# Kernel optimization log

Hardware: AMD Instinct MI355X
Metric: run time of the kernel (lower is better)

The kernel has to match this reference:

```python
import jax, jax.numpy as jnp
import numpy as np
from jax import lax

HEADS = 8
DIM_HEAD = 64
INNER = HEADS * DIM_HEAD  # 512
LOG_SCALE_MAX = float(np.log(100.0))  # clamp for clamp_exp (SwinV2-style max temperature 1/0.01)
EPS_NORM = 1e-12  # F.normalize eps
EPS_LN = 1e-5


def setup_inputs() -> dict:
    key = jax.random.key(0)
    ks = jax.random.split(key, 6)
    b, c, h, w = 2, 256, 48, 48
    x = jax.random.normal(ks[0], (b, c, h, w), jnp.float32)
    w_in = jax.random.normal(ks[1], (3 * INNER, c), jnp.float32) * (c ** -0.5)
    b_in = jnp.zeros((3 * INNER,), jnp.float32)
    # learnable log-scale, init log(d_head ** -0.5), per head
    softmax_scale = jnp.full((HEADS, 1, 1), float(np.log(DIM_HEAD ** -0.5)), jnp.float32)
    w_dw = jax.random.normal(ks[2], (INNER, 1, 3, 3), jnp.float32) * (1.0 / 3.0)
    w_pw = jax.random.normal(ks[3], (2 * c, INNER), jnp.float32) * (INNER ** -0.5)
    gamma = jnp.full((2 * c,), 1e-3, jnp.float32)  # norm init_weight=0.001
    beta = jnp.zeros((2 * c,), jnp.float32)
    return {"x": x, "w_in": w_in, "b_in": b_in, "softmax_scale": softmax_scale,
            "w_dw": w_dw, "w_pw": w_pw, "gamma": gamma, "beta": beta}


def _l2norm(t):
    n = jnp.sqrt(jnp.sum(t * t, axis=-1, keepdims=True))
    return t / jnp.maximum(n, EPS_NORM)


def reference(x, w_in, b_in, softmax_scale, w_dw, w_pw, gamma, beta):
    b, c, h, w = x.shape
    s = h * w
    # proj_in: 1x1 conv then 'b (h c) x y -> b h x y c'
    y = jnp.einsum('bchw,oc->bohw', x, w_in) + b_in[None, :, None, None]
    y = y.reshape(b, HEADS, 3 * DIM_HEAD, h, w).transpose(0, 1, 3, 4, 2)  # b H x y (3*dh)
    y = y.reshape(b, HEADS, s, 3 * DIM_HEAD)
    q, k, v = jnp.split(y, 3, axis=-1)  # each [b, H, s, dh]
    # scaled cosine attention
    qn, kn = _l2norm(q), _l2norm(k)
    scale = jnp.exp(jnp.minimum(softmax_scale, LOG_SCALE_MAX))  # clamp_exp, [H,1,1]
    sim = jnp.einsum('bhid,bhjd->bhij', qn, kn) * scale[None]
    attn = jax.nn.softmax(sim, axis=-1)
    out = jnp.einsum('bhij,bhjd->bhid', attn, v)  # [b,H,s,dh]
    # unsplit heads -> 'b (h w) c' -> 'b c h w'
    update = out.transpose(0, 2, 1, 3).reshape(b, s, INNER)
    update = update.transpose(0, 2, 1).reshape(b, INNER, h, w)
    # proj_out: depthwise 3x3 (no bias) + pointwise 1x1 (no bias)
    dw = lax.conv_general_dilated(update, w_dw, (1, 1), 'SAME',
                                  feature_group_count=INNER,
                                  dimension_numbers=('NCHW', 'OIHW', 'NCHW'))
    pw = jnp.einsum('bchw,oc->bohw', dw, w_pw)  # [b, 2c, h, w]
    # channelwise layernorm with small init weight (norm_scales_and_shifts)
    mu = jnp.mean(pw, axis=1, keepdims=True)
    var = jnp.var(pw, axis=1, keepdims=True)
    normed = (pw - mu) * lax.rsqrt(var + EPS_LN)
    normed = normed * gamma[None, :, None, None] + beta[None, :, None, None]
    scales, shifts = jnp.split(normed, 2, axis=1)  # each [b, c, h, w]
    return shifts + x * scales
```

## Files before the change

### kernel.cpp

```cpp
#include <hip/hip_runtime.h>

#define B_ 2
#define C_ 256
#define S_ 2304
#define DH_ 64
#define O3_ 1536
#define INNER_ 512
#define LOGSMAX 4.605170185988092f
#define LOG2E 1.4426950408889634f

typedef __attribute__((ext_vector_type(8))) short short8;
typedef __attribute__((ext_vector_type(4))) float f32x4;
typedef __attribute__((ext_vector_type(16))) float f32x16;
typedef __attribute__((ext_vector_type(4))) unsigned short us4;
typedef __attribute__((ext_vector_type(2))) unsigned u32x2;
typedef __attribute__((ext_vector_type(4))) unsigned u32x4;
typedef __bf16 bf16x8 __attribute__((ext_vector_type(8)));

__device__ __forceinline__ unsigned short f2bf(float f) {
  unsigned u = __builtin_bit_cast(unsigned, f);
  u += 0x7FFFu + ((u >> 16) & 1u);
  return (unsigned short)(u >> 16);
}
__device__ __forceinline__ float bf2f(unsigned short h) {
  return __builtin_bit_cast(float, (unsigned)h << 16);
}
__device__ __forceinline__ bf16x8 as_bf(short8 v) {
  return __builtin_bit_cast(bf16x8, v);
}
__device__ __forceinline__ float fexp2(float x) {
#if __has_builtin(__builtin_amdgcn_exp2f)
  return __builtin_amdgcn_exp2f(x);
#else
  return __expf(x * 0.6931471805599453f);
#endif
}
__device__ __forceinline__ float frcp(float x) {
#if __has_builtin(__builtin_amdgcn_rcpf)
  return __builtin_amdgcn_rcpf(x);
#else
  return 1.f / x;
#endif
}
__device__ __forceinline__ unsigned pack_hi16(unsigned b, unsigned a) {
  return __builtin_amdgcn_perm(b, a, 0x07060302u);
}
__device__ __forceinline__ unsigned pack_lo16(unsigned b, unsigned a) {
  return __builtin_amdgcn_perm(b, a, 0x05040100u);
}

__global__ __launch_bounds__(256) void k_prep(const float* __restrict__ x,
                                              const float* __restrict__ w_in,
                                              const float* __restrict__ w_pw,
                                              unsigned short* __restrict__ xT,
                                              unsigned short* __restrict__ w_inb,
                                              unsigned short* __restrict__ w_pwb) {
  __shared__ float tile[64][65];
  int blk = blockIdx.x;
  int t = threadIdx.x;
  if (blk < 288) {
    int p0 = (blk % 36) * 64, c0 = ((blk / 36) % 4) * 64, b = blk / 144;
    const float* xb = x + (size_t)b * C_ * S_;
#pragma unroll
    for (int i = 0; i < 16; i++) {
      int c = i * 4 + (t >> 6);
      int p = t & 63;
      tile[c][p] = xb[(size_t)(c0 + c) * S_ + p0 + p];
    }
    __syncthreads();
    unsigned short* xTb = xT + (size_t)b * S_ * C_;
#pragma unroll
    for (int i = 0; i < 16; i++) {
      int p = i * 4 + (t >> 6);
      int c = t & 63;
      xTb[(size_t)(p0 + p) * C_ + c0 + c] = f2bf(tile[c][p]);
    }
  } else if (blk < 288 + 1536) {
    int i = (blk - 288) * 256 + t;
    w_inb[i] = f2bf(w_in[i]);
  } else {
    int i = (blk - 1824) * 256 + t;
    w_pwb[i] = f2bf(w_pw[i]);
  }
}

__global__ __launch_bounds__(256) void k_gemm_qkv(const unsigned short* __restrict__ A,
                                                  const unsigned short* __restrict__ BT,
                                                  const float* __restrict__ b_in,
                                                  const float* __restrict__ ss,
                                                  unsigned char* __restrict__ qn,
                                                  unsigned char* __restrict__ kn,
                                                  unsigned short* __restrict__ vv) {
  __shared__ __align__(16) unsigned short As[64][72];
  __shared__ __align__(16) unsigned short Bs[128][72];
  int t = threadIdx.x;
  int lane = t & 63, wv = t >> 6;
  int quad = lane >> 4, r15 = lane & 15;
  int by = blockIdx.y;
  int m0 = by * 64, n0 = blockIdx.x * 128;
  int b = blockIdx.z;
  const unsigned short* BTb = BT + (size_t)b * S_ * C_;

  f32x4 acc[4][2] = {};

  int srA = t >> 2, scA = (t & 3) * 16;
  int srB = t >> 1, scB = (t & 1) * 32;
  const unsigned short* ag = A + (size_t)(m0 + srA) * C_ + scA;
  const unsigned short* bg = BTb + (size_t)(n0 + srB) * C_ + scB;

  for (int k0 = 0; k0 < C_; k0 += 64) {
    short8 a0 = *(const short8*)(ag + k0);
    short8 a1 = *(const short8*)(ag + k0 + 8);
    short8 b0 = *(const short8*)(bg + k0);
    short8 b1 = *(const short8*)(bg + k0 + 8);
    short8 b2 = *(const short8*)(bg + k0 + 16);
    short8 b3 = *(const short8*)(bg + k0 + 24);
    __syncthreads();
    *(short8*)&As[srA][scA] = a0;
    *(short8*)&As[srA][scA + 8] = a1;
    *(short8*)&Bs[srB][scB] = b0;
    *(short8*)&Bs[srB][scB + 8] = b1;
    *(short8*)&Bs[srB][scB + 16] = b2;
    *(short8*)&Bs[srB][scB + 24] = b3;
    __syncthreads();
#pragma unroll
    for (int ks = 0; ks < 2; ks++) {
      short8 af[4], bfr[2];
#pragma unroll
      for (int i = 0; i < 4; i++) af[i] = *(const short8*)&As[i * 16 + r15][ks * 32 + quad * 8];
#pragma unroll
      for (int j = 0; j < 2; j++) bfr[j] = *(const short8*)&Bs[wv * 32 + j * 16 + r15][ks * 32 + quad * 8];
#pragma unroll
      for (int i = 0; i < 4; i++)
#pragma unroll
        for (int j = 0; j < 2; j++)
          acc[i][j] = __builtin_amdgcn_mfma_f32_16x16x32_bf16(as_bf(af[i]), as_bf(bfr[j]), acc[i][j], 0, 0, 0);
    }
  }

  int h = by / 3, seg = by - h * 3;
  int bh = b * 8 + h;
  f32x4 bi[4];
#pragma unroll
  for (int i = 0; i < 4; i++) bi[i] = *(const f32x4*)&b_in[m0 + i * 16 + quad * 4];
  float bv[4][2][4];
  float ssq0 = 0.f, ssq1 = 0.f;
#pragma unroll
  for (int i = 0; i < 4; i++)
#pragma unroll
    for (int rr = 0; rr < 4; rr++) {
      float v0 = acc[i][0][rr] + bi[i][rr];
      float v1 = acc[i][1][rr] + bi[i][rr];
      bv[i][0][rr] = v0;
      bv[i][1][rr] = v1;
      ssq0 += v0 * v0;
      ssq1 += v1 * v1;
    }
  if (seg < 2) {
    float sc = (seg == 0) ? __expf(fminf(ss[h], LOGSMAX)) * LOG2E : 1.f;
    ssq0 += __shfl_xor(ssq0, 16);
    ssq0 += __shfl_xor(ssq0, 32);
    ssq1 += __shfl_xor(ssq1, 16);
    ssq1 += __shfl_xor(ssq1, 32);
    float inv0 = sc / fmaxf(sqrtf(ssq0), 1e-12f);
    float inv1 = sc / fmaxf(sqrtf(ssq1), 1e-12f);
    unsigned char* dst = (seg == 0 ? qn : kn) + (size_t)bh * S_ * DH_;
#pragma unroll
    for (int i = 0; i < 4; i++)
#pragma unroll
      for (int j = 0; j < 2; j++) {
        float iv = j ? inv1 : inv0;
        int pk = __builtin_amdgcn_cvt_pk_fp8_f32(bv[i][j][0] * iv, bv[i][j][1] * iv, 0, false);
        pk = __builtin_amdgcn_cvt_pk_fp8_f32(bv[i][j][2] * iv, bv[i][j][3] * iv, pk, true);
        int p = n0 + wv * 32 + j * 16 + r15;
        *(int*)&dst[(size_t)p * DH_ + i * 16 + quad * 4] = pk;
      }
  } else {
    unsigned short* dst = vv + (size_t)bh * S_ * DH_;
#pragma unroll
    for (int i = 0; i < 4; i++)
#pragma unroll
      for (int j = 0; j < 2; j++) {
        us4 o = {f2bf(bv[i][j][0]), f2bf(bv[i][j][1]), f2bf(bv[i][j][2]), f2bf(bv[i][j][3])};
        int p = n0 + wv * 32 + j * 16 + r15;
        *(us4*)&dst[(size_t)p * DH_ + i * 16 + quad * 4] = o;
      }
  }
}

__global__ __launch_bounds__(128) void k_gemm2(const unsigned short* __restrict__ A,
                                               const unsigned short* __restrict__ BT,
                                               float* __restrict__ outp,
                                               int M, int N, int K) {
  __shared__ __align__(16) unsigned short As[64][72];
  __shared__ __align__(16) unsigned short Bs[64][72];
  int t = threadIdx.x;
  int lane = t & 63, wv = t >> 6;
  int quad = lane >> 4, r15 = lane & 15;
  int m0 = blockIdx.y * 64, n0 = blockIdx.x * 64;
  int b = blockIdx.z;
  const unsigned short* BTb = BT + (size_t)b * N * K;

  f32x4 acc[4][2] = {};

  int sr = t >> 1, sc = (t & 1) * 32;
  const unsigned short* ag = A + (size_t)(m0 + sr) * K + sc;
  const unsigned short* bg = BTb + (size_t)(n0 + sr) * K + sc;

  for (int k0 = 0; k0 < K; k0 += 64) {
    short8 a0 = *(const short8*)(ag + k0);
    short8 a1 = *(const short8*)(ag + k0 + 8);
    short8 a2 = *(const short8*)(ag + k0 + 16);
    short8 a3 = *(const short8*)(ag + k0 + 24);
    short8 b0 = *(const short8*)(bg + k0);
    short8 b1 = *(const short8*)(bg + k0 + 8);
    short8 b2 = *(const short8*)(bg + k0 + 16);
    short8 b3 = *(const short8*)(bg + k0 + 24);
    __syncthreads();
    *(short8*)&As[sr][sc] = a0;
    *(short8*)&As[sr][sc + 8] = a1;
    *(short8*)&As[sr][sc + 16] = a2;
    *(short8*)&As[sr][sc + 24] = a3;
    *(short8*)&Bs[sr][sc] = b0;
    *(short8*)&Bs[sr][sc + 8] = b1;
    *(short8*)&Bs[sr][sc + 16] = b2;
    *(short8*)&Bs[sr][sc + 24] = b3;
    __syncthreads();
#pragma unroll
    for (int ks = 0; ks < 2; ks++) {
      short8 af[4], bfr[2];
#pragma unroll
      for (int i = 0; i < 4; i++) af[i] = *(const short8*)&As[i * 16 + r15][ks * 32 + quad * 8];
#pragma unroll
      for (int j = 0; j < 2; j++) bfr[j] = *(const short8*)&Bs[wv * 32 + j * 16 + r15][ks * 32 + quad * 8];
#pragma unroll
      for (int i = 0; i < 4; i++)
#pragma unroll
        for (int j = 0; j < 2; j++)
          acc[i][j] = __builtin_amdgcn_mfma_f32_16x16x32_bf16(as_bf(af[i]), as_bf(bfr[j]), acc[i][j], 0, 0, 0);
    }
  }
  float* Cb = outp + (size_t)b * M * N;
#pragma unroll
  for (int i = 0; i < 4; i++)
#pragma unroll
    for (int j = 0; j < 2; j++)
#pragma unroll
      for (int rr = 0; rr < 4; rr++) {
        int row = m0 + i * 16 + quad * 4 + rr;
        int col = n0 + wv * 32 + j * 16 + r15;
        Cb[(size_t)row * N + col] = acc[i][j][rr];
      }
}

__global__ __launch_bounds__(256) void k_attn(const unsigned char* __restrict__ qn,
                                              const unsigned char* __restrict__ kn,
                                              const unsigned short* __restrict__ vv,
                                              const float* __restrict__ ss,
                                              unsigned short* __restrict__ attnp,
                                              float* __restrict__ lp) {
  __shared__ __align__(16) unsigned char Ks[64][72];
  __shared__ __align__(16) unsigned short Vs[64][72];
  __shared__ __align__(16) unsigned short Ps[4][32][76];
  int t = threadIdx.x;
  int w = t >> 6;
  int lane = t & 63;
  int l31 = lane & 31, hi = lane >> 5;
  int bh = blockIdx.x;
  int q0 = blockIdx.y * 128 + w * 32;
  int split = blockIdx.z;
  int ktbase = split * 12;
  const unsigned char* qb = qn + (size_t)bh * S_ * DH_;
  const unsigned char* kb = kn + (size_t)bh * S_ * DH_;
  const unsigned short* vb = vv + (size_t)bh * S_ * DH_;
  float shift2 = __expf(fminf(ss[bh & 7], LOGSMAX)) * LOG2E;

  const unsigned char* qrow = qb + (size_t)(q0 + l31) * DH_ + hi * 8;
  long qf[4];
#pragma unroll
  for (int ks = 0; ks < 4; ks++) qf[ks] = *(const long*)(qrow + ks * 16);

  const f32x16 z16 = {};
  f32x16 O0 = z16, O1 = z16;
  float l_part = 0.f;

  int srow = t >> 2;
  int scol = (t & 3) * 16;
  const unsigned char* kg = kb + ((size_t)(ktbase * 64) + srow) * DH_ + scol;

  int dp = w * 8 + ((t & 63) >> 3);
  int koct = t & 7;
  const unsigned* vg32 = (const unsigned*)vb + ((size_t)(ktbase * 64 + koct * 8)) * 32 + dp;

  uint4 kr = *(const uint4*)kg;
  unsigned lv[8];
#pragma unroll
  for (int kk = 0; kk < 8; kk++) lv[kk] = vg32[(size_t)kk * 32];

  for (int i = 0; i < 12; i++) {
    __syncthreads();
    *(uint4*)&Ks[srow][scol] = kr;
    {
      u32x4 ev = {pack_lo16(lv[1], lv[0]), pack_lo16(lv[3], lv[2]),
                  pack_lo16(lv[5], lv[4]), pack_lo16(lv[7], lv[6])};
      u32x4 od = {pack_hi16(lv[1], lv[0]), pack_hi16(lv[3], lv[2]),
                  pack_hi16(lv[5], lv[4]), pack_hi16(lv[7], lv[6])};
      *(u32x4*)&Vs[2 * dp][koct * 8] = ev;
      *(u32x4*)&Vs[2 * dp + 1][koct * 8] = od;
    }
    __syncthreads();
    if (i < 11) {
      kr = *(const uint4*)(kg + (size_t)(i + 1) * 64 * DH_);
      const unsigned* vg = vg32 + (size_t)(i + 1) * 64 * 32;
#pragma unroll
      for (int kk = 0; kk < 8; kk++) lv[kk] = vg[(size_t)kk * 32];
    }
    f32x16 sc0, sc1;
    {
      long a0 = *(const long*)&Ks[l31][hi * 8];
      long a1 = *(const long*)&Ks[32 + l31][hi * 8];
      sc0 = __builtin_amdgcn_mfma_f32_32x32x16_fp8_fp8(a0, qf[0], z16, 0, 0, 0);
      sc1 = __builtin_amdgcn_mfma_f32_32x32x16_fp8_fp8(a1, qf[0], z16, 0, 0, 0);
    }
#pragma unroll
    for (int ks = 1; ks < 4; ks++) {
      long a0 = *(const long*)&Ks[l31][ks * 16 + hi * 8];
      long a1 = *(const long*)&Ks[32 + l31][ks * 16 + hi * 8];
      sc0 = __builtin_amdgcn_mfma_f32_32x32x16_fp8_fp8(a0, qf[ks], sc0, 0, 0, 0);
      sc1 = __builtin_amdgcn_mfma_f32_32x32x16_fp8_fp8(a1, qf[ks], sc1, 0, 0, 0);
    }
    float lsum = 0.f;
#pragma unroll
    for (int mt = 0; mt < 2; mt++) {
      const f32x16& s = mt ? sc1 : sc0;
#pragma unroll
      for (int g = 0; g < 4; g++) {
        float e0 = fexp2(s[g * 4 + 0] - shift2);
        float e1 = fexp2(s[g * 4 + 1] - shift2);
        float e2 = fexp2(s[g * 4 + 2] - shift2);
        float e3 = fexp2(s[g * 4 + 3] - shift2);
        lsum += (e0 + e1) + (e2 + e3);
        unsigned u0 = __builtin_bit_cast(unsigned, e0) + 0x8000u;
        unsigned u1 = __builtin_bit_cast(unsigned, e1) + 0x8000u;
        unsigned u2 = __builtin_bit_cast(unsigned, e2) + 0x8000u;
        unsigned u3 = __builtin_bit_cast(unsigned, e3) + 0x8000u;
        u32x2 pk = {pack_hi16(u1, u0), pack_hi16(u3, u2)};
        *(u32x2*)&Ps[w][l31][mt * 32 + g * 8 + hi * 4] = pk;
      }
    }
    l_part += lsum;
#pragma unroll
    for (int ks = 0; ks < 4; ks++) {
      short8 pb = *(const short8*)&Ps[w][l31][ks * 16 + hi * 8];
      short8 va0 = *(const short8*)&Vs[l31][ks * 16 + hi * 8];
      short8 va1 = *(const short8*)&Vs[32 + l31][ks * 16 + hi * 8];
      O0 = __builtin_amdgcn_mfma_f32_32x32x16_bf16(as_bf(va0), as_bf(pb), O0, 0, 0, 0);
      O1 = __builtin_amdgcn_mfma_f32_32x32x16_bf16(as_bf(va1), as_bf(pb), O1, 0, 0, 0);
    }
  }
  float l = l_part + __shfl_xor(l_part, 32);
  if (hi == 0) lp[((size_t)(split * 16 + bh)) * S_ + q0 + l31] = l;
  unsigned short* orow = attnp + (((size_t)(split * 16 + bh)) * S_ + q0 + l31) * DH_;
#pragma unroll
  for (int mt = 0; mt < 2; mt++) {
    const f32x16& O = mt ? O1 : O0;
#pragma unroll
    for (int g = 0; g < 4; g++) {
      us4 o4 = {f2bf(O[g * 4 + 0]), f2bf(O[g * 4 + 1]), f2bf(O[g * 4 + 2]), f2bf(O[g * 4 + 3])};
      *(us4*)&orow[mt * 32 + g * 8 + hi * 4] = o4;
    }
  }
}

__global__ __launch_bounds__(256) void k_dwconv(const unsigned short* __restrict__ attnp,
                                                const float* __restrict__ lp,
                                                const float* __restrict__ w_dw,
                                                unsigned short* __restrict__ dwb) {
  int t = threadIdx.x;
  int d = t & 63;
  int pj = t >> 6;
  int p = blockIdx.y * 4 + pj;
  int bh = blockIdx.x;
  int b = bh >> 3, h = bh & 7;
  int yy = p / 48, xx = p % 48;
  const unsigned short* a0 = attnp + (size_t)bh * S_ * DH_ + d;
  const unsigned short* a1 = attnp + ((size_t)(16 + bh)) * S_ * DH_ + d;
  const unsigned short* a2 = attnp + ((size_t)(32 + bh)) * S_ * DH_ + d;
  const float* l0 = lp + (size_t)bh * S_;
  const float* l1 = lp + (size_t)(16 + bh) * S_;
  const float* l2 = lp + (size_t)(32 + bh) * S_;
  int ch = h * 64 + d;
  float w[9];
#pragma unroll
  for (int i = 0; i < 9; i++) w[i] = w_dw[ch * 9 + i];
  float acc = 0.f;
#pragma unroll
  for (int dy = -1; dy <= 1; dy++) {
    int y2 = yy + dy;
    if (y2 < 0 || y2 >= 48) continue;
#pragma unroll
    for (int dx = -1; dx <= 1; dx++) {
      int x2 = xx + dx;
      if (x2 < 0 || x2 >= 48) continue;
      int p2 = y2 * 48 + x2;
      float rl = frcp(l0[p2] + l1[p2] + l2[p2]);
      float v = (bf2f(a0[(size_t)p2 * DH_]) + bf2f(a1[(size_t)p2 * DH_]) + bf2f(a2[(size_t)p2 * DH_])) * rl;
      acc += v * w[(dy + 1) * 3 + dx + 1];
    }
  }
  dwb[((size_t)b * S_ + p) * INNER_ + ch] = f2bf(acc);
}

__global__ __launch_bounds__(256) void k_ln_final(const float* __restrict__ pw,
                                                  const float* __restrict__ gamma,
                                                  const float* __restrict__ beta,
                                                  const float* __restrict__ x,
                                                  float* __restrict__ out) {
  __shared__ float s_s0[32][8], s_s1[32][8], s_q0[32][8], s_q1[32][8];
  int t = threadIdx.x;
  int pl = t & 7, g = t >> 3;
  int b = blockIdx.y;
  int p = blockIdx.x * 16 + pl * 2;
  const float* pwb = pw + (size_t)b * INNER_ * S_ + p;
  float s0 = 0.f, s1 = 0.f, q0 = 0.f, q1 = 0.f;
#pragma unroll
  for (int j = 0; j < 16; j++) {
    float2 v = *(const float2*)&pwb[(size_t)(g * 16 + j) * S_];
    s0 += v.x; s1 += v.y;
    q0 += v.x * v.x; q1 += v.y * v.y;
  }
  s_s0[g][pl] = s0; s_s1[g][pl] = s1;
  s_q0[g][pl] = q0; s_q1[g][pl] = q1;
  __syncthreads();
  float t0 = 0.f, t1 = 0.f, u0 = 0.f, u1 = 0.f;
#pragma unroll
  for (int i = 0; i < 32; i++) {
    t0 += s_s0[i][pl]; t1 += s_s1[i][pl];
    u0 += s_q0[i][pl]; u1 += s_q1[i][pl];
  }
  float mu0 = t0 * (1.f / 512.f), mu1 = t1 * (1.f / 512.f);
  float rs0 = rsqrtf(u0 * (1.f / 512.f) - mu0 * mu0 + 1e-5f);
  float rs1 = rsqrtf(u1 * (1.f / 512.f) - mu1 * mu1 + 1e-5f);
  const float* xb = x + (size_t)b * C_ * S_ + p;
  float* ob = out + (size_t)b * C_ * S_ + p;
#pragma unroll
  for (int j = 0; j < 8; j++) {
    int cc = g * 8 + j;
    float ga = gamma[cc], be = beta[cc];
    float gs = gamma[cc + 256], bs = beta[cc + 256];
    float2 pv = *(const float2*)&pwb[(size_t)cc * S_];
    float2 sv = *(const float2*)&pwb[(size_t)(cc + 256) * S_];
    float2 xv = *(const float2*)&xb[(size_t)cc * S_];
    float sc0 = (pv.x - mu0) * rs0 * ga + be;
    float sc1 = (pv.y - mu1) * rs1 * ga + be;
    float sh0 = (sv.x - mu0) * rs0 * gs + bs;
    float sh1 = (sv.y - mu1) * rs1 * gs + bs;
    float2 o;
    o.x = sh0 + xv.x * sc0;
    o.y = sh1 + xv.y * sc1;
    *(float2*)&ob[(size_t)cc * S_] = o;
  }
}

extern "C" void kernel_launch(void* const* d_in, const int* in_sizes, int n_in,
                              void* d_out, int out_size, void* d_ws, size_t ws_size,
                              hipStream_t stream) {
  const float* x = (const float*)d_in[0];
  const float* w_in = (const float*)d_in[1];
  const float* b_in = (const float*)d_in[2];
  const float* ss = (const float*)d_in[3];
  const float* w_dw = (const float*)d_in[4];
  const float* w_pw = (const float*)d_in[5];
  const float* gamma = (const float*)d_in[6];
  const float* beta = (const float*)d_in[7];
  float* out = (float*)d_out;
  char* ws = (char*)d_ws;

  unsigned short* xT = (unsigned short*)(ws + 0);
  unsigned short* w_inb = (unsigned short*)(ws + 2359296);
  unsigned short* w_pwb = (unsigned short*)(ws + 3145728);
  unsigned char* qn = (unsigned char*)(ws + 3670016);
  unsigned char* kn = (unsigned char*)(ws + 6029312);
  unsigned short* vv = (unsigned short*)(ws + 8388608);
  unsigned short* dwb = (unsigned short*)(ws + 13107200);
  float* lp = (float*)(ws + 17825792);
  unsigned short* attnp = (unsigned short*)(ws + 18268160);
  float* pw = (float*)(ws + 32423936);

  k_prep<<<2848, 256, 0, stream>>>(x, w_in, w_pw, xT, w_inb, w_pwb);
  k_gemm_qkv<<<dim3(18, 24, 2), 256, 0, stream>>>(w_inb, xT, b_in, ss, qn, kn, vv);
  k_attn<<<dim3(16, 18, 3), 256, 0, stream>>>(qn, kn, vv, ss, attnp, lp);
  k_dwconv<<<dim3(16, 576), 256, 0, stream>>>(attnp, lp, w_dw, dwb);
  k_gemm2<<<dim3(36, 8, 2), 128, 0, stream>>>(w_pwb, dwb, pw, INNER_, S_, INNER_);
  k_ln_final<<<dim3(144, 2), 256, 0, stream>>>(pw, gamma, beta, x, out);
}
```

Baseline: 165.7 us.

## Fuse weight bf16 conversion into GEMMs, keep P in registers, split keys four ways

The separate bf16 conversion of w_in and w_pw is dropped from the prep kernel; each GEMM now loads the fp32 weights and packs them to bf16 on the fly. In the attention kernel the softmax probabilities no longer pass through LDS: they are packed in registers and rearranged with cross-lane shuffles to form the MFMA B operand. The key dimension is also split into 4 chunks instead of 3, and dwconv sums four partials. The change trades extra fp32 weight traffic in the GEMMs for less LDS work and more parallel blocks, at the cost of one more partial buffer to write and reduce.

```diff
diff --git a/kernel.cpp b/kernel.cpp
--- a/kernel.cpp
+++ b/kernel.cpp
@@ -48,43 +48,36 @@
 __device__ __forceinline__ unsigned pack_lo16(unsigned b, unsigned a) {
   return __builtin_amdgcn_perm(b, a, 0x05040100u);
 }
+__device__ __forceinline__ unsigned pk2(float a, float b) {
+  unsigned ua = __builtin_bit_cast(unsigned, a) + 0x8000u;
+  unsigned ub = __builtin_bit_cast(unsigned, b) + 0x8000u;
+  return pack_hi16(ub, ua);
+}
 
 __global__ __launch_bounds__(256) void k_prep(const float* __restrict__ x,
-                                              const float* __restrict__ w_in,
-                                              const float* __restrict__ w_pw,
-                                              unsigned short* __restrict__ xT,
-                                              unsigned short* __restrict__ w_inb,
-                                              unsigned short* __restrict__ w_pwb) {
+                                              unsigned short* __restrict__ xT) {
   __shared__ float tile[64][65];
   int blk = blockIdx.x;
   int t = threadIdx.x;
-  if (blk < 288) {
-    int p0 = (blk % 36) * 64, c0 = ((blk / 36) % 4) * 64, b = blk / 144;
-    const float* xb = x + (size_t)b * C_ * S_;
-#pragma unroll
-    for (int i = 0; i < 16; i++) {
-      int c = i * 4 + (t >> 6);
-      int p = t & 63;
-      tile[c][p] = xb[(size_t)(c0 + c) * S_ + p0 + p];
-    }
-    __syncthreads();
-    unsigned short* xTb = xT + (size_t)b * S_ * C_;
-#pragma unroll
-    for (int i = 0; i < 16; i++) {
-      int p = i * 4 + (t >> 6);
-      int c = t & 63;
-      xTb[(size_t)(p0 + p) * C_ + c0 + c] = f2bf(tile[c][p]);
-    }
-  } else if (blk < 288 + 1536) {
-    int i = (blk - 288) * 256 + t;
-    w_inb[i] = f2bf(w_in[i]);
-  } else {
-    int i = (blk - 1824) * 256 + t;
-    w_pwb[i] = f2bf(w_pw[i]);
-  }
-}
-
-__global__ __launch_bounds__(256) void k_gemm_qkv(const unsigned short* __restrict__ A,
+  int p0 = (blk % 36) * 64, c0 = ((blk / 36) % 4) * 64, b = blk / 144;
+  const float* xb = x + (size_t)b * C_ * S_;
+#pragma unroll
+  for (int i = 0; i < 16; i++) {
+    int c = i * 4 + (t >> 6);
+    int p = t & 63;
+    tile[c][p] = xb[(size_t)(c0 + c) * S_ + p0 + p];
+  }
+  __syncthreads();
+  unsigned short* xTb = xT + (size_t)b * S_ * C_;
+#pragma unroll
+  for (int i = 0; i < 16; i++) {
+    int p = i * 4 + (t >> 6);
+    int c = t & 63;
+    xTb[(size_t)(p0 + p) * C_ + c0 + c] = f2bf(tile[c][p]);
+  }
+}
+
+__global__ __launch_bounds__(256) void k_gemm_qkv(const float* __restrict__ w_in,
                                                   const unsigned short* __restrict__ BT,
                                                   const float* __restrict__ b_in,
                                                   const float* __restrict__ ss,
@@ -105,19 +98,23 @@
 
   int srA = t >> 2, scA = (t & 3) * 16;
   int srB = t >> 1, scB = (t & 1) * 32;
-  const unsigned short* ag = A + (size_t)(m0 + srA) * C_ + scA;
+  const float* agf = w_in + (size_t)(m0 + srA) * C_ + scA;
   const unsigned short* bg = BTb + (size_t)(n0 + srB) * C_ + scB;
 
   for (int k0 = 0; k0 < C_; k0 += 64) {
-    short8 a0 = *(const short8*)(ag + k0);
-    short8 a1 = *(const short8*)(ag + k0 + 8);
+    f32x4 f0 = *(const f32x4*)(agf + k0);
+    f32x4 f1 = *(const f32x4*)(agf + k0 + 4);
+    f32x4 f2 = *(const f32x4*)(agf + k0 + 8);
+    f32x4 f3 = *(const f32x4*)(agf + k0 + 12);
     short8 b0 = *(const short8*)(bg + k0);
     short8 b1 = *(const short8*)(bg + k0 + 8);
     short8 b2 = *(const short8*)(bg + k0 + 16);
     short8 b3 = *(const short8*)(bg + k0 + 24);
+    u32x4 alo = {pk2(f0[0], f0[1]), pk2(f0[2], f0[3]), pk2(f1[0], f1[1]), pk2(f1[2], f1[3])};
+    u32x4 ahi = {pk2(f2[0], f2[1]), pk2(f2[2], f2[3]), pk2(f3[0], f3[1]), pk2(f3[2], f3[3])};
     __syncthreads();
-    *(short8*)&As[srA][scA] = a0;
-    *(short8*)&As[srA][scA + 8] = a1;
+    *(u32x4*)&As[srA][scA] = alo;
+    *(u32x4*)&As[srA][scA + 8] = ahi;
     *(short8*)&Bs[srB][scB] = b0;
     *(short8*)&Bs[srB][scB + 8] = b1;
     *(short8*)&Bs[srB][scB + 16] = b2;
@@ -188,7 +185,7 @@
   }
 }
 
-__global__ __launch_bounds__(128) void k_gemm2(const unsigned short* __restrict__ A,
+__global__ __launch_bounds__(128) void k_gemm2(const float* __restrict__ w_pw,
                                                const unsigned short* __restrict__ BT,
                                                float* __restrict__ outp,
                                                int M, int N, int K) {
@@ -204,23 +201,26 @@
   f32x4 acc[4][2] = {};
 
   int sr = t >> 1, sc = (t & 1) * 32;
-  const unsigned short* ag = A + (size_t)(m0 + sr) * K + sc;
+  const float* agf = w_pw + (size_t)(m0 + sr) * K + sc;
   const unsigned short* bg = BTb + (size_t)(n0 + sr) * K + sc;
 
   for (int k0 = 0; k0 < K; k0 += 64) {
-    short8 a0 = *(const short8*)(ag + k0);
-    short8 a1 = *(const short8*)(ag + k0 + 8);
-    short8 a2 = *(const short8*)(ag + k0 + 16);
-    short8 a3 = *(const short8*)(ag + k0 + 24);
+    f32x4 f[8];
+#pragma unroll
+    for (int i = 0; i < 8; i++) f[i] = *(const f32x4*)(agf + k0 + i * 4);
     short8 b0 = *(const short8*)(bg + k0);
     short8 b1 = *(const short8*)(bg + k0 + 8);
     short8 b2 = *(const short8*)(bg + k0 + 16);
     short8 b3 = *(const short8*)(bg + k0 + 24);
+    u32x4 a01 = {pk2(f[0][0], f[0][1]), pk2(f[0][2], f[0][3]), pk2(f[1][0], f[1][1]), pk2(f[1][2], f[1][3])};
+    u32x4 a23 = {pk2(f[2][0], f[2][1]), pk2(f[2][2], f[2][3]), pk2(f[3][0], f[3][1]), pk2(f[3][2], f[3][3])};
+    u32x4 a45 = {pk2(f[4][0], f[4][1]), pk2(f[4][2], f[4][3]), pk2(f[5][0], f[5][1]), pk2(f[5][2], f[5][3])};
+    u32x4 a67 = {pk2(f[6][0], f[6][1]), pk2(f[6][2], f[6][3]), pk2(f[7][0], f[7][1]), pk2(f[7][2], f[7][3])};
     __syncthreads();
-    *(short8*)&As[sr][sc] = a0;
-    *(short8*)&As[sr][sc + 8] = a1;
-    *(short8*)&As[sr][sc + 16] = a2;
-    *(short8*)&As[sr][sc + 24] = a3;
+    *(u32x4*)&As[sr][sc] = a01;
+    *(u32x4*)&As[sr][sc + 8] = a23;
+    *(u32x4*)&As[sr][sc + 16] = a45;
+    *(u32x4*)&As[sr][sc + 24] = a67;
     *(short8*)&Bs[sr][sc] = b0;
     *(short8*)&Bs[sr][sc + 8] = b1;
     *(short8*)&Bs[sr][sc + 16] = b2;
@@ -261,7 +261,6 @@
                                               float* __restrict__ lp) {
   __shared__ __align__(16) unsigned char Ks[64][72];
   __shared__ __align__(16) unsigned short Vs[64][72];
-  __shared__ __align__(16) unsigned short Ps[4][32][76];
   int t = threadIdx.x;
   int w = t >> 6;
   int lane = t & 63;
@@ -269,7 +268,7 @@
   int bh = blockIdx.x;
   int q0 = blockIdx.y * 128 + w * 32;
   int split = blockIdx.z;
-  int ktbase = split * 12;
+  int ktbase = split * 9;
   const unsigned char* qb = qn + (size_t)bh * S_ * DH_;
   const unsigned char* kb = kn + (size_t)bh * S_ * DH_;
   const unsigned short* vb = vv + (size_t)bh * S_ * DH_;
@@ -297,7 +296,7 @@
 #pragma unroll
   for (int kk = 0; kk < 8; kk++) lv[kk] = vg32[(size_t)kk * 32];
 
-  for (int i = 0; i < 12; i++) {
+  for (int i = 0; i < 9; i++) {
     __syncthreads();
     *(uint4*)&Ks[srow][scol] = kr;
     {
@@ -309,7 +308,7 @@
       *(u32x4*)&Vs[2 * dp + 1][koct * 8] = od;
     }
     __syncthreads();
-    if (i < 11) {
+    if (i < 8) {
       kr = *(const uint4*)(kg + (size_t)(i + 1) * 64 * DH_);
       const unsigned* vg = vg32 + (size_t)(i + 1) * 64 * 32;
 #pragma unroll
@@ -329,33 +328,41 @@
       sc0 = __builtin_amdgcn_mfma_f32_32x32x16_fp8_fp8(a0, qf[ks], sc0, 0, 0, 0);
       sc1 = __builtin_amdgcn_mfma_f32_32x32x16_fp8_fp8(a1, qf[ks], sc1, 0, 0, 0);
     }
-    float lsum = 0.f;
 #pragma unroll
     for (int mt = 0; mt < 2; mt++) {
       const f32x16& s = mt ? sc1 : sc0;
-#pragma unroll
-      for (int g = 0; g < 4; g++) {
-        float e0 = fexp2(s[g * 4 + 0] - shift2);
-        float e1 = fexp2(s[g * 4 + 1] - shift2);
-        float e2 = fexp2(s[g * 4 + 2] - shift2);
-        float e3 = fexp2(s[g * 4 + 3] - shift2);
+      unsigned pk[8];
+      float lsum = 0.f;
+#pragma unroll
+      for (int g2 = 0; g2 < 4; g2++) {
+        float e0 = fexp2(s[g2 * 4 + 0] - shift2);
+        float e1 = fexp2(s[g2 * 4 + 1] - shift2);
+        float e2 = fexp2(s[g2 * 4 + 2] - shift2);
+        float e3 = fexp2(s[g2 * 4 + 3] - shift2);
         lsum += (e0 + e1) + (e2 + e3);
-        unsigned u0 = __builtin_bit_cast(unsigned, e0) + 0x8000u;
-        unsigned u1 = __builtin_bit_cast(unsigned, e1) + 0x8000u;
-        unsigned u2 = __builtin_bit_cast(unsigned, e2) + 0x8000u;
-        unsigned u3 = __builtin_bit_cast(unsigned, e3) + 0x8000u;
-        u32x2 pk = {pack_hi16(u1, u0), pack_hi16(u3, u2)};
-        *(u32x2*)&Ps[w][l31][mt * 32 + g * 8 + hi * 4] = pk;
+        pk[2 * g2] = pk2(e0, e1);
+        pk[2 * g2 + 1] = pk2(e2, e3);
       }
-    }
-    l_part += lsum;
-#pragma unroll
-    for (int ks = 0; ks < 4; ks++) {
-      short8 pb = *(const short8*)&Ps[w][l31][ks * 16 + hi * 8];
-      short8 va0 = *(const short8*)&Vs[l31][ks * 16 + hi * 8];
-      short8 va1 = *(const short8*)&Vs[32 + l31][ks * 16 + hi * 8];
-      O0 = __builtin_amdgcn_mfma_f32_32x32x16_bf16(as_bf(va0), as_bf(pb), O0, 0, 0, 0);
-      O1 = __builtin_amdgcn_mfma_f32_32x32x16_bf16(as_bf(va1), as_bf(pb), O1, 0, 0, 0);
+      l_part += lsum;
+#pragma unroll
+      for (int half = 0; half < 2; half++) {
+        int gb = half * 4;
+        unsigned ya = hi ? pk[gb + 0] : pk[gb + 2];
+        unsigned yb = hi ? pk[gb + 1] : pk[gb + 3];
+        unsigned ra = __shfl_xor(ya, 32);
+        unsigned rb = __shfl_xor(yb, 32);
+        u32x4 fd;
+        fd[0] = hi ? ra : pk[gb + 0];
+        fd[1] = hi ? rb : pk[gb + 1];
+        fd[2] = hi ? pk[gb + 2] : ra;
+        fd[3] = hi ? pk[gb + 3] : rb;
+        short8 pb = __builtin_bit_cast(short8, fd);
+        int ks = mt * 2 + half;
+        short8 va0 = *(const short8*)&Vs[l31][ks * 16 + hi * 8];
+        short8 va1 = *(const short8*)&Vs[32 + l31][ks * 16 + hi * 8];
+        O0 = __builtin_amdgcn_mfma_f32_32x32x16_bf16(as_bf(va0), as_bf(pb), O0, 0, 0, 0);
+        O1 = __builtin_amdgcn_mfma_f32_32x32x16_bf16(as_bf(va1), as_bf(pb), O1, 0, 0, 0);
+      }
     }
   }
   float l = l_part + __shfl_xor(l_part, 32);
@@ -386,9 +393,11 @@
   const unsigned short* a0 = attnp + (size_t)bh * S_ * DH_ + d;
   const unsigned short* a1 = attnp + ((size_t)(16 + bh)) * S_ * DH_ + d;
   const unsigned short* a2 = attnp + ((size_t)(32 + bh)) * S_ * DH_ + d;
+  const unsigned short* a3 = attnp + ((size_t)(48 + bh)) * S_ * DH_ + d;
   const float* l0 = lp + (size_t)bh * S_;
   const float* l1 = lp + (size_t)(16 + bh) * S_;
   const float* l2 = lp + (size_t)(32 + bh) * S_;
+  const float* l3 = lp + (size_t)(48 + bh) * S_;
   int ch = h * 64 + d;
   float w[9];
 #pragma unroll
@@ -403,8 +412,9 @@
       int x2 = xx + dx;
       if (x2 < 0 || x2 >= 48) continue;
       int p2 = y2 * 48 + x2;
-      float rl = frcp(l0[p2] + l1[p2] + l2[p2]);
-      float v = (bf2f(a0[(size_t)p2 * DH_]) + bf2f(a1[(size_t)p2 * DH_]) + bf2f(a2[(size_t)p2 * DH_])) * rl;
+      float rl = frcp(l0[p2] + l1[p2] + l2[p2] + l3[p2]);
+      float v = (bf2f(a0[(size_t)p2 * DH_]) + bf2f(a1[(size_t)p2 * DH_]) +
+                 bf2f(a2[(size_t)p2 * DH_]) + bf2f(a3[(size_t)p2 * DH_])) * rl;
       acc += v * w[(dy + 1) * 3 + dx + 1];
     }
   }
@@ -477,20 +487,18 @@
   char* ws = (char*)d_ws;
 
   unsigned short* xT = (unsigned short*)(ws + 0);
-  unsigned short* w_inb = (unsigned short*)(ws + 2359296);
-  unsigned short* w_pwb = (unsigned short*)(ws + 3145728);
-  unsigned char* qn = (unsigned char*)(ws + 3670016);
-  unsigned char* kn = (unsigned char*)(ws + 6029312);
-  unsigned short* vv = (unsigned short*)(ws + 8388608);
-  unsigned short* dwb = (unsigned short*)(ws + 13107200);
-  float* lp = (float*)(ws + 17825792);
-  unsigned short* attnp = (unsigned short*)(ws + 18268160);
-  float* pw = (float*)(ws + 32423936);
-
-  k_prep<<<2848, 256, 0, stream>>>(x, w_in, w_pw, xT, w_inb, w_pwb);
-  k_gemm_qkv<<<dim3(18, 24, 2), 256, 0, stream>>>(w_inb, xT, b_in, ss, qn, kn, vv);
-  k_attn<<<dim3(16, 18, 3), 256, 0, stream>>>(qn, kn, vv, ss, attnp, lp);
+  unsigned char* qn = (unsigned char*)(ws + 2359296);
+  unsigned char* kn = (unsigned char*)(ws + 4718592);
+  unsigned short* vv = (unsigned short*)(ws + 7077888);
+  unsigned short* dwb = (unsigned short*)(ws + 11796480);
+  float* lp = (float*)(ws + 16515072);
+  unsigned short* attnp = (unsigned short*)(ws + 17104896);
+  float* pw = (float*)(ws + 35979264);
+
+  k_prep<<<288, 256, 0, stream>>>(x, xT);
+  k_gemm_qkv<<<dim3(18, 24, 2), 256, 0, stream>>>(w_in, xT, b_in, ss, qn, kn, vv);
+  k_attn<<<dim3(16, 18, 4), 256, 0, stream>>>(qn, kn, vv, ss, attnp, lp);
   k_dwconv<<<dim3(16, 576), 256, 0, stream>>>(attnp, lp, w_dw, dwb);
-  k_gemm2<<<dim3(36, 8, 2), 128, 0, stream>>>(w_pwb, dwb, pw, INNER_, S_, INNER_);
+  k_gemm2<<<dim3(36, 8, 2), 128, 0, stream>>>(w_pw, dwb, pw, INNER_, S_, INNER_);
   k_ln_final<<<dim3(144, 2), 256, 0, stream>>>(pw, gamma, beta, x, out);
 }
```

After: 176.8 us. 6.7% more time.
